# Optimization experiments

Hardware: AMD Instinct MI355X
Metric: run time of the kernel (lower is better)

Reference implementation:

```python
import jax, jax.numpy as jnp
import numpy as np

N_SRC = 50000      # columns of adj / rows of x
N_SAMP = 50000     # rows of adj (sampled nodes this layer)
N_TOTAL = 200000   # rows of historical embedding buffer
E = 1600000        # nnz of adj
D_IN = 256
D_OUT = 256


def setup_inputs() -> dict:
    key = jax.random.key(0)
    ks = jax.random.split(key, 10)
    x = jax.random.normal(ks[0], (N_SRC, D_IN), dtype=jnp.float32)
    adj_row = jax.random.randint(ks[1], (E,), 0, N_SAMP, dtype=jnp.int32)
    adj_col = jax.random.randint(ks[2], (E,), 0, N_SRC, dtype=jnp.int32)
    adj_val = jax.random.uniform(ks[3], (E,), dtype=jnp.float32)
    nodes_per_layer = jax.random.randint(ks[4], (N_SAMP,), 0, N_TOTAL, dtype=jnp.int32)
    y_buf = jax.random.normal(ks[5], (N_TOTAL, D_IN), dtype=jnp.float32)
    W = jax.random.normal(ks[6], (D_IN, D_OUT), dtype=jnp.float32) / np.sqrt(D_IN)
    b = jax.random.normal(ks[7], (D_OUT,), dtype=jnp.float32) * 0.01
    scale = jnp.ones((D_OUT,), dtype=jnp.float32)
    offset = jnp.zeros((D_OUT,), dtype=jnp.float32)
    return {"x": x, "adj_row": adj_row, "adj_col": adj_col, "adj_val": adj_val,
            "nodes_per_layer": nodes_per_layer, "y_buf": y_buf,
            "W": W, "b": b, "scale": scale, "offset": offset}


def reference(x, adj_row, adj_col, adj_val, nodes_per_layer, y_buf, W, b, scale, offset):
    # ---- sparse aggregation: feat = spmm(adj, x)  [N_SAMP, D_IN]
    msgs = adj_val[:, None] * x[adj_col]                         # [E, D_IN]
    feat = jax.ops.segment_sum(msgs, adj_row, num_segments=N_SAMP)
    # ---- momentum blend with historical embeddings (training path)
    feat = 0.9 * y_buf[nodes_per_layer] + 0.1 * feat
    # buffer update: sampled rows <- feat.detach(); all other rows *= 0.9
    new_y = (y_buf * 0.9).at[nodes_per_layer].set(jax.lax.stop_gradient(feat))
    # ---- linear -> ELU -> custom per-row normalization
    out = jax.nn.elu(feat @ W + b)                               # [N_SAMP, D_OUT]
    mean = out.mean(axis=1, keepdims=True)
    var = out.var(axis=1, keepdims=True) + 1e-9                  # unbiased=False
    out = (out - mean) * scale * jax.lax.rsqrt(var) + offset
    return out, new_y
```

## Files before the change

kernel.cpp:

```cpp
#include <hip/hip_runtime.h>
#include <hip/hip_fp16.h>
#include <math.h>

#define N_SRC   50000
#define N_SAMP  50000
#define N_TOTAL 200000
#define NE      1600000
#define D       256

#define CBSHIFT 12
#define NB      13
#define NCELL   (N_SAMP * NB)

typedef unsigned short ushort;
typedef unsigned int   uint;
using bf16x8 = __attribute__((ext_vector_type(8))) short;
using f32x4v = __attribute__((ext_vector_type(4))) float;

__device__ __forceinline__ float4 ntload4(const float* p) {
    f32x4v t = __builtin_nontemporal_load((const f32x4v*)p);
    return make_float4(t.x, t.y, t.z, t.w);
}
__device__ __forceinline__ void ntstore4(float* p, float4 v) {
    f32x4v t; t.x = v.x; t.y = v.y; t.z = v.z; t.w = v.w;
    __builtin_nontemporal_store(t, (f32x4v*)p);
}

__device__ __forceinline__ ushort bf16_rne(float f) {
    uint u = __float_as_uint(f);
    uint r = u + 0x7FFFu + ((u >> 16) & 1u);
    return (ushort)(r >> 16);
}
__device__ __forceinline__ float bf16_tof(ushort h) {
    return __uint_as_float(((uint)h) << 16);
}

__device__ __forceinline__ float4 xload4h(const __half* p) {
    int2 r = *(const int2*)p;
    __half2 h0 = *(__half2*)&r.x;
    __half2 h1 = *(__half2*)&r.y;
    float2 f0 = __half22float2(h0);
    float2 f1 = __half22float2(h1);
    return make_float4(f0.x, f0.y, f1.x, f1.y);
}

__global__ __launch_bounds__(256) void k_init(
    int* __restrict__ cellcnt, int* __restrict__ owner, int* __restrict__ gtotal)
{
    int i = blockIdx.x * 256 + threadIdx.x;
    if (i < NCELL)   cellcnt[i] = 0;
    if (i < N_TOTAL) owner[i]   = -1;
    if (i == 0)      *gtotal    = 0;
}

__global__ __launch_bounds__(256) void k_prep(
    const float* __restrict__ x, __half* __restrict__ xh)
{
    int i = blockIdx.x * 256 + threadIdx.x;
    if (i >= (N_SRC * D) / 8) return;
    const float4* p = (const float4*)x + (size_t)i * 2;
    float4 a = p[0], c = p[1];
    __half2 h0 = __floats2half2_rn(a.x, a.y);
    __half2 h1 = __floats2half2_rn(a.z, a.w);
    __half2 h2 = __floats2half2_rn(c.x, c.y);
    __half2 h3 = __floats2half2_rn(c.z, c.w);
    int4 w;
    w.x = *(int*)&h0; w.y = *(int*)&h1; w.z = *(int*)&h2; w.w = *(int*)&h3;
    *(int4*)(xh + (size_t)i * 8) = w;
}

__global__ __launch_bounds__(256) void k_wsplit(
    const float* __restrict__ W, ushort* __restrict__ Wt_hi, ushort* __restrict__ Wt_lo)
{
    int idx = blockIdx.x * 256 + threadIdx.x;
    if (idx >= D * D) return;
    int k = idx >> 8;
    int n = idx & 255;
    float f = W[idx];
    ushort h = bf16_rne(f);
    ushort l = bf16_rne(f - bf16_tof(h));
    Wt_hi[n * D + k] = h;
    Wt_lo[n * D + k] = l;
}

__global__ __launch_bounds__(256) void k_count(
    const int* __restrict__ adj_row, const int* __restrict__ adj_col,
    const int* __restrict__ nodes, int* __restrict__ cellcnt, int* __restrict__ owner)
{
    int idx = blockIdx.x * 256 + threadIdx.x;
    if (idx < NE) {
        int row = adj_row[idx];
        int col = adj_col[idx];
        atomicAdd(&cellcnt[row * NB + (col >> CBSHIFT)], 1);
    }
    if (idx < N_SAMP) {
        atomicMax(&owner[nodes[idx]], idx);
    }
}

__global__ __launch_bounds__(256) void k_rowalloc(
    const int* __restrict__ cellcnt, int* __restrict__ cellcur,
    int* __restrict__ rowptr, int* __restrict__ rowcnt, int* __restrict__ gtotal)
{
    int r = blockIdx.x * 256 + threadIdx.x;
    if (r >= N_SAMP) return;
    int pref[NB];
    int sum = 0;
    #pragma unroll
    for (int cb = 0; cb < NB; ++cb) {
        pref[cb] = sum;
        sum += cellcnt[r * NB + cb];
    }
    int base = atomicAdd(gtotal, sum);
    rowptr[r] = base;
    rowcnt[r] = sum;
    #pragma unroll
    for (int cb = 0; cb < NB; ++cb)
        cellcur[r * NB + cb] = base + pref[cb];
}

__global__ __launch_bounds__(256) void k_scatter(
    const int* __restrict__ adj_row, const int* __restrict__ adj_col,
    const float* __restrict__ adj_val, int* __restrict__ cellcur, int2* __restrict__ bucket)
{
    int idx = blockIdx.x * 256 + threadIdx.x;
    if (idx >= NE) return;
    int row = adj_row[idx];
    int col = adj_col[idx];
    float val = adj_val[idx];
    int pos = atomicAdd(&cellcur[row * NB + (col >> CBSHIFT)], 1);
    bucket[pos] = make_int2(col, __float_as_int(val));
}

__global__ __launch_bounds__(256) void k_spmm_blend(
    const __half* __restrict__ xh, const int2* __restrict__ bucket,
    const int* __restrict__ rowptr, const int* __restrict__ rowcnt,
    const int* __restrict__ nodes, const int* __restrict__ owner,
    const float* __restrict__ y_buf, float* __restrict__ feat, float* __restrict__ newy)
{
    int wave = threadIdx.x >> 6;
    int lane = threadIdx.x & 63;
    int row  = blockIdx.x * 4 + wave;
    int off  = lane * 4;

    int cnt = rowcnt[row];
    const int2* bk = bucket + rowptr[row];
    float4 acc = make_float4(0.f, 0.f, 0.f, 0.f);
    int j = 0;
    for (; j + 3 < cnt; j += 4) {
        int2 e0 = bk[j],     e1 = bk[j + 1];
        int2 e2 = bk[j + 2], e3 = bk[j + 3];
        float v0 = __int_as_float(e0.y), v1 = __int_as_float(e1.y);
        float v2 = __int_as_float(e2.y), v3 = __int_as_float(e3.y);
        float4 x0 = xload4h(xh + (size_t)e0.x * D + off);
        float4 x1 = xload4h(xh + (size_t)e1.x * D + off);
        float4 x2 = xload4h(xh + (size_t)e2.x * D + off);
        float4 x3 = xload4h(xh + (size_t)e3.x * D + off);
        acc.x += v0 * x0.x + v1 * x1.x + v2 * x2.x + v3 * x3.x;
        acc.y += v0 * x0.y + v1 * x1.y + v2 * x2.y + v3 * x3.y;
        acc.z += v0 * x0.z + v1 * x1.z + v2 * x2.z + v3 * x3.z;
        acc.w += v0 * x0.w + v1 * x1.w + v2 * x2.w + v3 * x3.w;
    }
    for (; j < cnt; ++j) {
        int2 e0 = bk[j];
        float v0 = __int_as_float(e0.y);
        float4 x0 = xload4h(xh + (size_t)e0.x * D + off);
        acc.x += v0 * x0.x; acc.y += v0 * x0.y;
        acc.z += v0 * x0.z; acc.w += v0 * x0.w;
    }
    int node = nodes[row];
    float4 yv = ntload4(y_buf + (size_t)node * D + off);
    float4 f;
    f.x = 0.9f * yv.x + 0.1f * acc.x;
    f.y = 0.9f * yv.y + 0.1f * acc.y;
    f.z = 0.9f * yv.z + 0.1f * acc.z;
    f.w = 0.9f * yv.w + 0.1f * acc.w;
    *(float4*)(feat + (size_t)row * D + off) = f;
    if (owner[node] == row)
        ntstore4(newy + (size_t)node * D + off, f);

    int base = row * 4;
    int4 ow = *(const int4*)&owner[base];
    #pragma unroll
    for (int k = 0; k < 4; ++k) {
        int o = (k == 0) ? ow.x : (k == 1) ? ow.y : (k == 2) ? ow.z : ow.w;
        if (o < 0) {
            int r = base + k;
            float4 y = ntload4(y_buf + (size_t)r * D + off);
            ntstore4(newy + (size_t)r * D + off,
                     make_float4(0.9f * y.x, 0.9f * y.y, 0.9f * y.z, 0.9f * y.w));
        }
    }
}

__global__ __launch_bounds__(256) void k_gemm_elu_norm(
    float* __restrict__ io, const ushort* __restrict__ Wt_hi,
    const ushort* __restrict__ Wt_lo, const float* __restrict__ b,
    const float* __restrict__ scale, const float* __restrict__ offset)
{
    __shared__ ushort Fhi[32][264], Flo[32][264];
    __shared__ ushort Wh[256][40],  Wl[256][40];
    __shared__ float  red[2][2][16][2];

    int tid  = threadIdx.x;
    int w    = tid >> 6;
    int l    = tid & 63;
    int g    = l >> 4;
    int c16  = l & 15;
    int mt   = w & 1;
    int nh   = w >> 1;
    int r0   = blockIdx.x * 32;

    {
        int m  = tid >> 3;
        int c0 = (tid & 7) * 32;
        int r  = r0 + m;
        #pragma unroll
        for (int i = 0; i < 8; ++i) {
            float4 v = (r < N_SAMP) ? ntload4(io + (size_t)r * D + c0 + i * 4)
                                    : make_float4(0.f, 0.f, 0.f, 0.f);
            ushort h0 = bf16_rne(v.x), h1 = bf16_rne(v.y);
            ushort h2 = bf16_rne(v.z), h3 = bf16_rne(v.w);
            ushort l0 = bf16_rne(v.x - bf16_tof(h0));
            ushort l1 = bf16_rne(v.y - bf16_tof(h1));
            ushort l2 = bf16_rne(v.z - bf16_tof(h2));
            ushort l3 = bf16_rne(v.w - bf16_tof(h3));
            int c = c0 + i * 4;
            uint2 ph, pl;
            ph.x = (uint)h0 | ((uint)h1 << 16); ph.y = (uint)h2 | ((uint)h3 << 16);
            pl.x = (uint)l0 | ((uint)l1 << 16); pl.y = (uint)l2 | ((uint)l3 << 16);
            *(uint2*)&Fhi[m][c] = ph;
            *(uint2*)&Flo[m][c] = pl;
        }
    }

    f32x4v acc[8];
    #pragma unroll
    for (int t = 0; t < 8; ++t) acc[t] = (f32x4v)(0.f);

    for (int kt8 = 0; kt8 < 8; ++kt8) {
        int kt = kt8 * 32;
        __syncthreads();
        {
            int n = tid;
            const int4* gh = (const int4*)(Wt_hi + (size_t)n * D + kt);
            const int4* gl = (const int4*)(Wt_lo + (size_t)n * D + kt);
            #pragma unroll
            for (int i = 0; i < 4; ++i) {
                *(int4*)&Wh[n][i * 8] = gh[i];
                *(int4*)&Wl[n][i * 8] = gl[i];
            }
        }
        __syncthreads();
        int arow = mt * 16 + c16;
        bf16x8 ah = *(const bf16x8*)&Fhi[arow][kt + g * 8];
        bf16x8 al = *(const bf16x8*)&Flo[arow][kt + g * 8];
        #pragma unroll
        for (int t = 0; t < 8; ++t) {
            int n = nh * 128 + t * 16 + c16;
            bf16x8 bh = *(const bf16x8*)&Wh[n][g * 8];
            bf16x8 bl = *(const bf16x8*)&Wl[n][g * 8];
            acc[t] = __builtin_amdgcn_mfma_f32_16x16x32_bf16(ah, bh, acc[t], 0, 0, 0);
            acc[t] = __builtin_amdgcn_mfma_f32_16x16x32_bf16(al, bh, acc[t], 0, 0, 0);
            acc[t] = __builtin_amdgcn_mfma_f32_16x16x32_bf16(ah, bl, acc[t], 0, 0, 0);
        }
    }

    float bcol[8], scol[8], ocol[8];
    #pragma unroll
    for (int t = 0; t < 8; ++t) {
        int c = nh * 128 + t * 16 + c16;
        bcol[t] = b[c]; scol[t] = scale[c]; ocol[t] = offset[c];
    }
    float s[4] = {0.f, 0.f, 0.f, 0.f};
    float q[4] = {0.f, 0.f, 0.f, 0.f};
    #pragma unroll
    for (int t = 0; t < 8; ++t) {
        #pragma unroll
        for (int j = 0; j < 4; ++j) {
            float o = acc[t][j] + bcol[t];
            o = o > 0.f ? o : expf(o) - 1.f;
            acc[t][j] = o;
            s[j] += o;
            q[j] += o * o;
        }
    }
    #pragma unroll
    for (int j = 0; j < 4; ++j) {
        #pragma unroll
        for (int d2 = 1; d2 < 16; d2 <<= 1) {
            s[j] += __shfl_xor(s[j], d2, 64);
            q[j] += __shfl_xor(q[j], d2, 64);
        }
    }
    if (c16 == 0) {
        #pragma unroll
        for (int j = 0; j < 4; ++j) {
            red[mt][nh][g * 4 + j][0] = s[j];
            red[mt][nh][g * 4 + j][1] = q[j];
        }
    }
    __syncthreads();
    #pragma unroll
    for (int j = 0; j < 4; ++j) {
        int rr = g * 4 + j;
        float S = red[mt][0][rr][0] + red[mt][1][rr][0];
        float Q = red[mt][0][rr][1] + red[mt][1][rr][1];
        float mean = S * (1.0f / 256.0f);
        float var  = Q * (1.0f / 256.0f) - mean * mean + 1e-9f;
        float rstd = rsqrtf(var);
        int r = r0 + mt * 16 + rr;
        if (r < N_SAMP) {
            #pragma unroll
            for (int t = 0; t < 8; ++t) {
                int c = nh * 128 + t * 16 + c16;
                io[(size_t)r * D + c] = (acc[t][j] - mean) * scol[t] * rstd + ocol[t];
            }
        }
    }
}

extern "C" void kernel_launch(void* const* d_in, const int* in_sizes, int n_in,
                              void* d_out, int out_size, void* d_ws, size_t ws_size,
                              hipStream_t stream) {
    const float* x       = (const float*)d_in[0];
    const int*   adj_row = (const int*)  d_in[1];
    const int*   adj_col = (const int*)  d_in[2];
    const float* adj_val = (const float*)d_in[3];
    const int*   nodes   = (const int*)  d_in[4];
    const float* y_buf   = (const float*)d_in[5];
    const float* Wm      = (const float*)d_in[6];
    const float* b       = (const float*)d_in[7];
    const float* scale   = (const float*)d_in[8];
    const float* offset  = (const float*)d_in[9];

    float* out  = (float*)d_out;
    float* newy = out + (size_t)N_SAMP * D;

    char*   ws      = (char*)d_ws;
    int*    cellcnt = (int*)(ws);
    int*    cellcur = (int*)(ws + 3  * 1024 * 1024);
    int*    rowptr  = (int*)(ws + 6  * 1024 * 1024);
    int*    rowcnt  = (int*)(ws + 6  * 1024 * 1024 + 256 * 1024);
    int*    gtotal  = (int*)(ws + 6  * 1024 * 1024 + 512 * 1024);
    int*    owner   = (int*)(ws + 7  * 1024 * 1024);
    ushort* Wt_hi   = (ushort*)(ws + 8 * 1024 * 1024);
    ushort* Wt_lo   = (ushort*)(ws + 8 * 1024 * 1024 + 256 * 1024);
    int2*   bucket  = (int2*)(ws + 9 * 1024 * 1024);
    __half* xh      = (__half*)(ws + 22 * 1024 * 1024);

    k_init    <<<(NCELL + 255) / 256,      256, 0, stream>>>(cellcnt, owner, gtotal);
    k_prep    <<<(N_SRC * D / 8 + 255) / 256, 256, 0, stream>>>(x, xh);
    k_wsplit  <<<(D * D + 255) / 256,      256, 0, stream>>>(Wm, Wt_hi, Wt_lo);
    k_count   <<<(NE + 255) / 256,         256, 0, stream>>>(adj_row, adj_col, nodes, cellcnt, owner);
    k_rowalloc<<<(N_SAMP + 255) / 256,     256, 0, stream>>>(cellcnt, cellcur, rowptr, rowcnt, gtotal);
    k_scatter <<<(NE + 255) / 256,         256, 0, stream>>>(adj_row, adj_col, adj_val, cellcur, bucket);
    k_spmm_blend<<<N_SAMP / 4, 256, 0, stream>>>(
        xh, bucket, rowptr, rowcnt, nodes, owner, y_buf, out, newy);
    k_gemm_elu_norm<<<(N_SAMP + 31) / 32, 256, 0, stream>>>(out, Wt_hi, Wt_lo, b, scale, offset);
}
```

Baseline: 837.0 us.

## Pack bucket entries to 32 bits, refine column bins, fuse setup kernels

Each CSR bucket entry is compressed from int2 to a single uint: a 16-bit column index plus the edge value rounded to fp16. Rows are padded to multiples of 4 so the SpMM can fetch four entries with one uint4 load. Column binning goes from 4096-wide bins to 2048-wide bins for better gather locality. The init, x-to-half conversion and W split kernels are fused into one launch, and some loads switch between nontemporal and regular. This cuts bucket traffic and launch overhead, at the cost of fp16 rounding of edge values and a larger cell-count array.

New measurement: 786.9 us. -6.0%, faster.

```diff
diff --git a/kernel.cpp b/kernel.cpp
--- a/kernel.cpp
+++ b/kernel.cpp
@@ -8,8 +8,8 @@
 #define NE      1600000
 #define D       256
 
-#define CBSHIFT 12
-#define NB      13
+#define CBSHIFT 11
+#define NB      25
 #define NCELL   (N_SAMP * NB)
 
 typedef unsigned short ushort;
@@ -44,43 +44,40 @@
     return make_float4(f0.x, f0.y, f1.x, f1.y);
 }
 
-__global__ __launch_bounds__(256) void k_init(
-    int* __restrict__ cellcnt, int* __restrict__ owner, int* __restrict__ gtotal)
+__device__ __forceinline__ void eunpack(uint e, int& col, float& val) {
+    col = (int)(e & 0xFFFFu);
+    val = __half2float(__ushort_as_half((ushort)(e >> 16)));
+}
+
+__global__ __launch_bounds__(256) void k_setup(
+    int* __restrict__ cellcnt, int* __restrict__ owner, int* __restrict__ gtotal,
+    const float* __restrict__ x, __half* __restrict__ xh,
+    const float* __restrict__ W, ushort* __restrict__ Wt_hi, ushort* __restrict__ Wt_lo)
 {
     int i = blockIdx.x * 256 + threadIdx.x;
     if (i < NCELL)   cellcnt[i] = 0;
     if (i < N_TOTAL) owner[i]   = -1;
     if (i == 0)      *gtotal    = 0;
-}
-
-__global__ __launch_bounds__(256) void k_prep(
-    const float* __restrict__ x, __half* __restrict__ xh)
-{
-    int i = blockIdx.x * 256 + threadIdx.x;
-    if (i >= (N_SRC * D) / 8) return;
-    const float4* p = (const float4*)x + (size_t)i * 2;
-    float4 a = p[0], c = p[1];
-    __half2 h0 = __floats2half2_rn(a.x, a.y);
-    __half2 h1 = __floats2half2_rn(a.z, a.w);
-    __half2 h2 = __floats2half2_rn(c.x, c.y);
-    __half2 h3 = __floats2half2_rn(c.z, c.w);
-    int4 w;
-    w.x = *(int*)&h0; w.y = *(int*)&h1; w.z = *(int*)&h2; w.w = *(int*)&h3;
-    *(int4*)(xh + (size_t)i * 8) = w;
-}
-
-__global__ __launch_bounds__(256) void k_wsplit(
-    const float* __restrict__ W, ushort* __restrict__ Wt_hi, ushort* __restrict__ Wt_lo)
-{
-    int idx = blockIdx.x * 256 + threadIdx.x;
-    if (idx >= D * D) return;
-    int k = idx >> 8;
-    int n = idx & 255;
-    float f = W[idx];
-    ushort h = bf16_rne(f);
-    ushort l = bf16_rne(f - bf16_tof(h));
-    Wt_hi[n * D + k] = h;
-    Wt_lo[n * D + k] = l;
+    if (i < (N_SRC * D) / 8) {
+        float4 a = ntload4(x + (size_t)i * 8);
+        float4 c = ntload4(x + (size_t)i * 8 + 4);
+        __half2 h0 = __floats2half2_rn(a.x, a.y);
+        __half2 h1 = __floats2half2_rn(a.z, a.w);
+        __half2 h2 = __floats2half2_rn(c.x, c.y);
+        __half2 h3 = __floats2half2_rn(c.z, c.w);
+        int4 w;
+        w.x = *(int*)&h0; w.y = *(int*)&h1; w.z = *(int*)&h2; w.w = *(int*)&h3;
+        *(int4*)(xh + (size_t)i * 8) = w;
+    }
+    if (i < D * D) {
+        int k = i >> 8;
+        int n = i & 255;
+        float f = W[i];
+        ushort h = bf16_rne(f);
+        ushort l = bf16_rne(f - bf16_tof(h));
+        Wt_hi[n * D + k] = h;
+        Wt_lo[n * D + k] = l;
+    }
 }
 
 __global__ __launch_bounds__(256) void k_count(
@@ -89,8 +86,8 @@
 {
     int idx = blockIdx.x * 256 + threadIdx.x;
     if (idx < NE) {
-        int row = adj_row[idx];
-        int col = adj_col[idx];
+        int row = __builtin_nontemporal_load(adj_row + idx);
+        int col = __builtin_nontemporal_load(adj_col + idx);
         atomicAdd(&cellcnt[row * NB + (col >> CBSHIFT)], 1);
     }
     if (idx < N_SAMP) {
@@ -111,7 +108,7 @@
         pref[cb] = sum;
         sum += cellcnt[r * NB + cb];
     }
-    int base = atomicAdd(gtotal, sum);
+    int base = atomicAdd(gtotal, (sum + 3) & ~3);
     rowptr[r] = base;
     rowcnt[r] = sum;
     #pragma unroll
@@ -121,19 +118,20 @@
 
 __global__ __launch_bounds__(256) void k_scatter(
     const int* __restrict__ adj_row, const int* __restrict__ adj_col,
-    const float* __restrict__ adj_val, int* __restrict__ cellcur, int2* __restrict__ bucket)
+    const float* __restrict__ adj_val, int* __restrict__ cellcur, uint* __restrict__ bucket)
 {
     int idx = blockIdx.x * 256 + threadIdx.x;
     if (idx >= NE) return;
-    int row = adj_row[idx];
-    int col = adj_col[idx];
-    float val = adj_val[idx];
+    int   row = __builtin_nontemporal_load(adj_row + idx);
+    int   col = __builtin_nontemporal_load(adj_col + idx);
+    float val = __builtin_nontemporal_load(adj_val + idx);
+    uint  e   = (uint)col | ((uint)__half_as_ushort(__float2half_rn(val)) << 16);
     int pos = atomicAdd(&cellcur[row * NB + (col >> CBSHIFT)], 1);
-    bucket[pos] = make_int2(col, __float_as_int(val));
+    bucket[pos] = e;
 }
 
 __global__ __launch_bounds__(256) void k_spmm_blend(
-    const __half* __restrict__ xh, const int2* __restrict__ bucket,
+    const __half* __restrict__ xh, const uint* __restrict__ bucket,
     const int* __restrict__ rowptr, const int* __restrict__ rowcnt,
     const int* __restrict__ nodes, const int* __restrict__ owner,
     const float* __restrict__ y_buf, float* __restrict__ feat, float* __restrict__ newy)
@@ -144,32 +142,32 @@
     int off  = lane * 4;
 
     int cnt = rowcnt[row];
-    const int2* bk = bucket + rowptr[row];
+    const uint* bk = bucket + rowptr[row];
     float4 acc = make_float4(0.f, 0.f, 0.f, 0.f);
     int j = 0;
     for (; j + 3 < cnt; j += 4) {
-        int2 e0 = bk[j],     e1 = bk[j + 1];
-        int2 e2 = bk[j + 2], e3 = bk[j + 3];
-        float v0 = __int_as_float(e0.y), v1 = __int_as_float(e1.y);
-        float v2 = __int_as_float(e2.y), v3 = __int_as_float(e3.y);
-        float4 x0 = xload4h(xh + (size_t)e0.x * D + off);
-        float4 x1 = xload4h(xh + (size_t)e1.x * D + off);
-        float4 x2 = xload4h(xh + (size_t)e2.x * D + off);
-        float4 x3 = xload4h(xh + (size_t)e3.x * D + off);
+        uint4 ev = *(const uint4*)(bk + j);
+        int c0, c1, c2, c3; float v0, v1, v2, v3;
+        eunpack(ev.x, c0, v0); eunpack(ev.y, c1, v1);
+        eunpack(ev.z, c2, v2); eunpack(ev.w, c3, v3);
+        float4 x0 = xload4h(xh + (size_t)c0 * D + off);
+        float4 x1 = xload4h(xh + (size_t)c1 * D + off);
+        float4 x2 = xload4h(xh + (size_t)c2 * D + off);
+        float4 x3 = xload4h(xh + (size_t)c3 * D + off);
         acc.x += v0 * x0.x + v1 * x1.x + v2 * x2.x + v3 * x3.x;
         acc.y += v0 * x0.y + v1 * x1.y + v2 * x2.y + v3 * x3.y;
         acc.z += v0 * x0.z + v1 * x1.z + v2 * x2.z + v3 * x3.z;
         acc.w += v0 * x0.w + v1 * x1.w + v2 * x2.w + v3 * x3.w;
     }
     for (; j < cnt; ++j) {
-        int2 e0 = bk[j];
-        float v0 = __int_as_float(e0.y);
-        float4 x0 = xload4h(xh + (size_t)e0.x * D + off);
+        int c0; float v0;
+        eunpack(bk[j], c0, v0);
+        float4 x0 = xload4h(xh + (size_t)c0 * D + off);
         acc.x += v0 * x0.x; acc.y += v0 * x0.y;
         acc.z += v0 * x0.z; acc.w += v0 * x0.w;
     }
     int node = nodes[row];
-    float4 yv = ntload4(y_buf + (size_t)node * D + off);
+    float4 yv = *(const float4*)(y_buf + (size_t)node * D + off);
     float4 f;
     f.x = 0.9f * yv.x + 0.1f * acc.x;
     f.y = 0.9f * yv.y + 0.1f * acc.y;
@@ -186,7 +184,7 @@
         int o = (k == 0) ? ow.x : (k == 1) ? ow.y : (k == 2) ? ow.z : ow.w;
         if (o < 0) {
             int r = base + k;
-            float4 y = ntload4(y_buf + (size_t)r * D + off);
+            float4 y = *(const float4*)(y_buf + (size_t)r * D + off);
             ntstore4(newy + (size_t)r * D + off,
                      make_float4(0.9f * y.x, 0.9f * y.y, 0.9f * y.z, 0.9f * y.w));
         }
@@ -217,7 +215,7 @@
         int r  = r0 + m;
         #pragma unroll
         for (int i = 0; i < 8; ++i) {
-            float4 v = (r < N_SAMP) ? ntload4(io + (size_t)r * D + c0 + i * 4)
+            float4 v = (r < N_SAMP) ? *(const float4*)(io + (size_t)r * D + c0 + i * 4)
                                     : make_float4(0.f, 0.f, 0.f, 0.f);
             ushort h0 = bf16_rne(v.x), h1 = bf16_rne(v.y);
             ushort h2 = bf16_rne(v.z), h3 = bf16_rne(v.w);
@@ -339,22 +337,22 @@
 
     char*   ws      = (char*)d_ws;
     int*    cellcnt = (int*)(ws);
-    int*    cellcur = (int*)(ws + 3  * 1024 * 1024);
-    int*    rowptr  = (int*)(ws + 6  * 1024 * 1024);
-    int*    rowcnt  = (int*)(ws + 6  * 1024 * 1024 + 256 * 1024);
-    int*    gtotal  = (int*)(ws + 6  * 1024 * 1024 + 512 * 1024);
-    int*    owner   = (int*)(ws + 7  * 1024 * 1024);
-    ushort* Wt_hi   = (ushort*)(ws + 8 * 1024 * 1024);
-    ushort* Wt_lo   = (ushort*)(ws + 8 * 1024 * 1024 + 256 * 1024);
-    int2*   bucket  = (int2*)(ws + 9 * 1024 * 1024);
-    __half* xh      = (__half*)(ws + 22 * 1024 * 1024);
-
-    k_init    <<<(NCELL + 255) / 256,      256, 0, stream>>>(cellcnt, owner, gtotal);
-    k_prep    <<<(N_SRC * D / 8 + 255) / 256, 256, 0, stream>>>(x, xh);
-    k_wsplit  <<<(D * D + 255) / 256,      256, 0, stream>>>(Wm, Wt_hi, Wt_lo);
-    k_count   <<<(NE + 255) / 256,         256, 0, stream>>>(adj_row, adj_col, nodes, cellcnt, owner);
-    k_rowalloc<<<(N_SAMP + 255) / 256,     256, 0, stream>>>(cellcnt, cellcur, rowptr, rowcnt, gtotal);
-    k_scatter <<<(NE + 255) / 256,         256, 0, stream>>>(adj_row, adj_col, adj_val, cellcur, bucket);
+    int*    cellcur = (int*)(ws + 5  * 1024 * 1024);
+    int*    rowptr  = (int*)(ws + 10 * 1024 * 1024);
+    int*    rowcnt  = (int*)(ws + 10 * 1024 * 1024 + 256 * 1024);
+    int*    gtotal  = (int*)(ws + 10 * 1024 * 1024 + 512 * 1024);
+    int*    owner   = (int*)(ws + 11 * 1024 * 1024);
+    ushort* Wt_hi   = (ushort*)(ws + 12 * 1024 * 1024);
+    ushort* Wt_lo   = (ushort*)(ws + 12 * 1024 * 1024 + 128 * 1024);
+    uint*   bucket  = (uint*)(ws + 13 * 1024 * 1024);
+    __half* xh      = (__half*)(ws + 20 * 1024 * 1024);
+
+    int setup_threads = (N_SRC * D) / 8;
+    k_setup   <<<(setup_threads + 255) / 256, 256, 0, stream>>>(
+        cellcnt, owner, gtotal, x, xh, Wm, Wt_hi, Wt_lo);
+    k_count   <<<(NE + 255) / 256,     256, 0, stream>>>(adj_row, adj_col, nodes, cellcnt, owner);
+    k_rowalloc<<<(N_SAMP + 255) / 256, 256, 0, stream>>>(cellcnt, cellcur, rowptr, rowcnt, gtotal);
+    k_scatter <<<(NE + 255) / 256,     256, 0, stream>>>(adj_row, adj_col, adj_val, cellcur, bucket);
     k_spmm_blend<<<N_SAMP / 4, 256, 0, stream>>>(
         xh, bucket, rowptr, rowcnt, nodes, owner, y_buf, out, newy);
     k_gemm_elu_norm<<<(N_SAMP + 31) / 32, 256, 0, stream>>>(out, Wt_hi, Wt_lo, b, scale, offset);
```
